# Performance work log

Hardware: AMD Instinct MI355X
Metric: run time of the kernel (lower is better)

The kernel has to match this reference:

```python
import jax, jax.numpy as jnp
import numpy as np

B, S, D, H = 2, 2048, 1024, 16
HD = D // H

def setup_inputs() -> dict:
    key = jax.random.key(0)
    ks = jax.random.split(key, 5)
    sc = 1.0 / np.sqrt(D)
    return {
        "x": jax.random.normal(ks[0], (B, S, D), dtype=jnp.float32),
        "Wq": jax.random.normal(ks[1], (D, D), dtype=jnp.float32) * sc,
        "bq": jnp.zeros((D,), jnp.float32),
        "Wk": jax.random.normal(ks[2], (D, D), dtype=jnp.float32) * sc,
        "bk": jnp.zeros((D,), jnp.float32),
        "Wv": jax.random.normal(ks[3], (D, D), dtype=jnp.float32) * sc,
        "bv": jnp.zeros((D,), jnp.float32),
        "Wo": jax.random.normal(ks[4], (D, D), dtype=jnp.float32) * sc,
        "bo": jnp.zeros((D,), jnp.float32),
    }

def reference(x, Wq, bq, Wk, bk, Wv, bv, Wo, bo):
    b, s, d = x.shape
    def proj(W, bias):
        # [B,S,D] -> [B,H,S,HD]
        return (x @ W + bias).reshape(b, s, H, HD).swapaxes(1, 2)
    q = proj(Wq, bq)
    k = proj(Wk, bk)
    v = proj(Wv, bv)
    # naive full attention, matching the module (materializes [B,H,S,S])
    logits = jnp.einsum("bhqd,bhkd->bhqk", q, k) / jnp.sqrt(jnp.float32(HD))
    attn = jax.nn.softmax(logits, axis=-1)
    vals = jnp.einsum("bhqk,bhkd->bhqd", attn, v)
    vals = vals.swapaxes(1, 2).reshape(b, s, d)
    return vals @ Wo + bo
```

## Files before the change

kernel.cpp:

```cpp
#include <hip/hip_runtime.h>

typedef unsigned short u16;
typedef __bf16 bf16x8 __attribute__((ext_vector_type(8)));
typedef __bf16 bf16x4 __attribute__((ext_vector_type(4)));
typedef float f32x4 __attribute__((ext_vector_type(4)));

#define SC2 0.18033688f

__device__ __forceinline__ u16 f2bf(float f) {
    union { float f; unsigned int i; } v;
    v.f = f;
    unsigned int u = v.i;
    return (u16)((u + 0x7fffu + ((u >> 16) & 1u)) >> 16);
}

__device__ __forceinline__ void dma16(const void* g, void* l) {
    __builtin_amdgcn_global_load_lds(
        (__attribute__((address_space(1))) void*)g,
        (__attribute__((address_space(3))) void*)l, 16, 0, 0);
}


__global__ __launch_bounds__(256) void cvt_w4(
    const float* __restrict__ W0, const float* __restrict__ W1,
    const float* __restrict__ W2, const float* __restrict__ W3,
    u16* __restrict__ out) {
    __shared__ u16 t[32][33];
    int z = blockIdx.z;
    const float* in = (z == 0) ? W0 : (z == 1) ? W1 : (z == 2) ? W2 : W3;
    u16* o = out + (size_t)z * 1048576;
    int bx = blockIdx.x * 32, by = blockIdx.y * 32;
    int tx = threadIdx.x & 31, ty = threadIdx.x >> 5;
#pragma unroll
    for (int i = 0; i < 32; i += 8)
        t[ty + i][tx] = f2bf(in[(size_t)(by + ty + i) * 1024 + bx + tx]);
    __syncthreads();
#pragma unroll
    for (int i = 0; i < 32; i += 8) {
        int n = bx + ty + i, k = by + tx;
        o[(size_t)n * 1024 + (k ^ ((n & 7) << 3))] = t[tx][ty + i];
    }
}

__global__ __launch_bounds__(256) void cvt_x(const float* __restrict__ in,
                                             u16* __restrict__ out) {
    int i = blockIdx.x * 256 + threadIdx.x;
    int s = i >> 8, k = (i & 255) * 4;
    float4 f = reinterpret_cast<const float4*>(in)[i];
    ushort4 h;
    h.x = f2bf(f.x); h.y = f2bf(f.y); h.z = f2bf(f.z); h.w = f2bf(f.w);
    *reinterpret_cast<ushort4*>(&out[(size_t)s * 1024 + (k ^ ((s & 7) << 3))]) = h;
}

__global__ __launch_bounds__(256) void gemm_qkv(
    const u16* __restrict__ xbf, const u16* __restrict__ wt,
    const float* __restrict__ bq, const float* __restrict__ bk,
    const float* __restrict__ bv,
    u16* __restrict__ qkg, u16* __restrict__ vgt) {
    __shared__ __align__(16) u16 As[128 * 64];
    __shared__ __align__(16) u16 Bs[128 * 64];

    int tid = threadIdx.x;
    int m0 = blockIdx.y * 128, n0 = blockIdx.x * 128;
    int wave = tid >> 6, lane = tid & 63;
    int wm = (wave >> 1) * 64, wn = (wave & 1) * 64;
    int l16 = lane & 15, quad = lane >> 4;
    int sl = l16 & 7;

    int seg = n0 >> 10;
    int n0r = n0 & 1023;
    const u16* WT = wt + (size_t)seg * 1048576;
    bool swp = (seg == 2);

    f32x4 acc[4][4];
#pragma unroll
    for (int mi = 0; mi < 4; mi++)
#pragma unroll
        for (int ni = 0; ni < 4; ni++) acc[mi][ni] = (f32x4){0.f, 0.f, 0.f, 0.f};

    int rsub = lane >> 3, c16 = (lane & 7) * 8;
    for (int k0 = 0; k0 < 1024; k0 += 64) {
#pragma unroll
        for (int i = 0; i < 4; i++) {
            int row = wave * 32 + i * 8 + rsub;
            dma16(&xbf[(size_t)(m0 + row) * 1024 + k0 + c16], &As[wave * 2048 + i * 512]);
            dma16(&WT[(size_t)(n0r + row) * 1024 + k0 + c16], &Bs[wave * 2048 + i * 512]);
        }
        __syncthreads();
        const u16* Am = swp ? Bs : As;
        const u16* Bn = swp ? As : Bs;
#pragma unroll
        for (int kk = 0; kk < 64; kk += 32) {
            int co = ((((kk >> 3) + quad) ^ sl) << 3);
            bf16x8 af[4], bf[4];
#pragma unroll
            for (int mi = 0; mi < 4; mi++)
                af[mi] = *reinterpret_cast<const bf16x8*>(
                    &Am[(wm + mi * 16 + l16) * 64 + co]);
#pragma unroll
            for (int ni = 0; ni < 4; ni++)
                bf[ni] = *reinterpret_cast<const bf16x8*>(
                    &Bn[(wn + ni * 16 + l16) * 64 + co]);
#pragma unroll
            for (int mi = 0; mi < 4; mi++)
#pragma unroll
                for (int ni = 0; ni < 4; ni++)
                    acc[mi][ni] = __builtin_amdgcn_mfma_f32_16x16x32_bf16(
                        af[mi], bf[ni], acc[mi][ni], 0, 0, 0);
        }
        __syncthreads();
    }

    if (!swp) {
        float sc = (seg == 0) ? SC2 : 1.0f;
#pragma unroll
        for (int ni = 0; ni < 4; ni++) {
            int n = n0 + wn + ni * 16 + l16;
            float bb = (n < 1024) ? bq[n] : bk[n - 1024];
#pragma unroll
            for (int mi = 0; mi < 4; mi++)
#pragma unroll
                for (int r = 0; r < 4; r++) {
                    int s = m0 + wm + mi * 16 + quad * 4 + r;
                    int key = (seg == 0) ? (s & 7) : ((s >> 2) & 7);
                    int col = n ^ (key << 3);
                    qkg[(size_t)(s >> 11) * 4194304 + (size_t)(s & 2047) * 2048 + col] =
                        f2bf((acc[mi][ni][r] + bb) * sc);
                }
        }
    } else {
#pragma unroll
        for (int mi = 0; mi < 4; mi++)
#pragma unroll
            for (int r = 0; r < 4; r++) {
                int v = n0r + wm + mi * 16 + quad * 4 + r;
                float bb = bv[v];
#pragma unroll
                for (int ni = 0; ni < 4; ni++) {
                    int s = m0 + wn + ni * 16 + l16;
                    int scol = (s & 2047) ^ ((v & 7) << 3);
                    vgt[(size_t)((s >> 11) * 1024 + v) * 2048 + scol] =
                        f2bf(acc[mi][ni][r] + bb);
                }
            }
    }
}

__global__ __launch_bounds__(512) void attention_kern(
    u16* __restrict__ qkg, const u16* __restrict__ vgt) {
    __shared__ __align__(16) u16 KsB[3][64 * 64];
    __shared__ __align__(16) u16 VtB[3][64 * 64];
    __shared__ __align__(16) u16 Ps[128 * 64];

    int tid = threadIdx.x;
    int bid = blockIdx.x;
    int id = (bid & 7) * 64 + (bid >> 3);
    int qt = id & 15, h = (id >> 4) & 15, b = id >> 8;

    int wave = tid >> 6, lane = tid & 63;
    int l16 = lane & 15, quad = lane >> 4;
    int rsub = lane >> 3, c16 = (lane & 7) * 8;
    int sl = l16 & 7;

    u16* qb = qkg + (size_t)b * 4194304 + (size_t)(qt * 128) * 2048 + h * 64;
    const u16* kb = qkg + (size_t)b * 4194304 + 1024 + h * 64;
    const u16* vb = vgt + (size_t)(b * 1024 + h * 64) * 2048;

    bf16x8 qf[2];
    {
        const u16* qr = qb + (size_t)(wave * 16 + l16) * 2048;
        qf[0] = *reinterpret_cast<const bf16x8*>(&qr[(quad ^ sl) << 3]);
        qf[1] = *reinterpret_cast<const bf16x8*>(&qr[((4 + quad) ^ sl) << 3]);
    }

    bf16x8 onef;
#pragma unroll
    for (int i = 0; i < 8; i++) onef[i] = (__bf16)1.0f;

    f32x4 o[4], ls;
#pragma unroll
    for (int ni = 0; ni < 4; ni++) o[ni] = (f32x4){0.f, 0.f, 0.f, 0.f};
    ls = (f32x4){0.f, 0.f, 0.f, 0.f};

    int r8 = wave * 8 + rsub;
    int gk = 4 * (r8 & 15) + (r8 >> 4);

    auto STAGE = [&](int kt, u16* kd, u16* vd) {
        const u16* ktb = kb + (size_t)(kt * 64) * 2048;
        const u16* vtb = vb + kt * 64;
        dma16(&ktb[(size_t)gk * 2048 + c16], kd + wave * 512);
        dma16(&vtb[(size_t)r8 * 2048 + c16], vd + wave * 512);
    };

    u16 *k0 = KsB[0], *k1 = KsB[1], *k2 = KsB[2];
    u16 *v0 = VtB[0], *v1 = VtB[1], *v2 = VtB[2];

    STAGE(0, k0, v0);

    for (int kt = 0; kt < 32; kt++) {
        if (kt < 31) {
            STAGE(kt + 1, k1, v1);
            asm volatile("s_waitcnt vmcnt(2) lgkmcnt(0)\n\ts_barrier" ::: "memory");
        } else {
            asm volatile("s_waitcnt vmcnt(0) lgkmcnt(0)\n\ts_barrier" ::: "memory");
        }

        f32x4 s[4];
#pragma unroll
        for (int ni = 0; ni < 4; ni++) s[ni] = (f32x4){0.f, 0.f, 0.f, 0.f};
#pragma unroll
        for (int kk = 0; kk < 64; kk += 32) {
            int co = ((((kk >> 3) + quad) ^ sl) << 3);
            bf16x8 af = qf[kk >> 5];
#pragma unroll
            for (int ni = 0; ni < 4; ni++) {
                bf16x8 bfr = *reinterpret_cast<const bf16x8*>(
                    &k0[(ni * 16 + l16) * 64 + co]);
                s[ni] = __builtin_amdgcn_mfma_f32_16x16x32_bf16(af, bfr, s[ni], 0, 0, 0);
            }
        }

#pragma unroll
        for (int r = 0; r < 4; r++) {
            f32x4 pf = {__builtin_amdgcn_exp2f(s[0][r]),
                        __builtin_amdgcn_exp2f(s[1][r]),
                        __builtin_amdgcn_exp2f(s[2][r]),
                        __builtin_amdgcn_exp2f(s[3][r])};
            bf16x4 pb = __builtin_convertvector(pf, bf16x4);
            int q = wave * 16 + quad * 4 + r;
            *reinterpret_cast<bf16x4*>(
                &Ps[q * 64 + (((l16 >> 1) ^ (q & 7)) << 3) + (l16 & 1) * 4]) = pb;
        }

#pragma unroll
        for (int kk = 0; kk < 64; kk += 32) {
            int co = ((((kk >> 3) + quad) ^ sl) << 3);
            bf16x8 af = *reinterpret_cast<const bf16x8*>(
                &Ps[(wave * 16 + l16) * 64 + co]);
            ls = __builtin_amdgcn_mfma_f32_16x16x32_bf16(af, onef, ls, 0, 0, 0);
#pragma unroll
            for (int ni = 0; ni < 4; ni++) {
                bf16x8 bfr = *reinterpret_cast<const bf16x8*>(
                    &v0[(ni * 16 + l16) * 64 + co]);
                o[ni] = __builtin_amdgcn_mfma_f32_16x16x32_bf16(af, bfr, o[ni], 0, 0, 0);
            }
        }

        u16* tk = k0; k0 = k1; k1 = k2; k2 = tk;
        u16* tv = v0; v0 = v1; v1 = v2; v2 = tv;
    }

    float inv[4];
#pragma unroll
    for (int r = 0; r < 4; r++) inv[r] = __builtin_amdgcn_rcpf(ls[r]);
#pragma unroll
    for (int ni = 0; ni < 4; ni++)
#pragma unroll
        for (int r = 0; r < 4; r++) {
            int s = qt * 128 + wave * 16 + quad * 4 + r;
            int d = h * 64 + ni * 16 + l16;
            qkg[(size_t)b * 4194304 + (size_t)s * 2048 + (d ^ ((s & 7) << 3))] =
                f2bf(o[ni][r] * inv[r]);
        }
}

__global__ __launch_bounds__(256) void gemm_out(
    const u16* __restrict__ attb, const u16* __restrict__ wot,
    const float* __restrict__ bo, float* __restrict__ out) {
    __shared__ __align__(16) u16 A3[3][128 * 64];
    __shared__ __align__(16) u16 B3[3][64 * 64];

    int tid = threadIdx.x;
    int m0 = blockIdx.y * 128, n0 = blockIdx.x * 64;
    int wave = tid >> 6, lane = tid & 63;
    int wm = (wave >> 1) * 64, wn = (wave & 1) * 32;
    int l16 = lane & 15, quad = lane >> 4;
    int sl = l16 & 7;
    int rsub = lane >> 3, c16 = (lane & 7) * 8;

    f32x4 acc[4][2];
#pragma unroll
    for (int mi = 0; mi < 4; mi++)
#pragma unroll
        for (int ni = 0; ni < 2; ni++) acc[mi][ni] = (f32x4){0.f, 0.f, 0.f, 0.f};

    auto STAGE = [&](int k0, u16* ad, u16* bd) {
#pragma unroll
        for (int i = 0; i < 4; i++) {
            int row = wave * 32 + i * 8 + rsub;
            dma16(&attb[(size_t)(m0 + row) * 2048 + k0 + c16], ad + wave * 2048 + i * 512);
        }
#pragma unroll
        for (int i = 0; i < 2; i++) {
            int row = wave * 16 + i * 8 + rsub;
            dma16(&wot[(size_t)(n0 + row) * 1024 + k0 + c16], bd + wave * 1024 + i * 512);
        }
    };

    u16 *a0 = A3[0], *a1 = A3[1], *a2 = A3[2];
    u16 *b0 = B3[0], *b1 = B3[1], *b2 = B3[2];

    STAGE(0, a0, b0);

    for (int k = 0; k < 16; k++) {
        if (k < 15) {
            STAGE((k + 1) * 64, a1, b1);
            asm volatile("s_waitcnt vmcnt(6) lgkmcnt(0)\n\ts_barrier" ::: "memory");
        } else {
            asm volatile("s_waitcnt vmcnt(0) lgkmcnt(0)\n\ts_barrier" ::: "memory");
        }
#pragma unroll
        for (int kk = 0; kk < 64; kk += 32) {
            int co = ((((kk >> 3) + quad) ^ sl) << 3);
            bf16x8 af[4], bf[2];
#pragma unroll
            for (int mi = 0; mi < 4; mi++)
                af[mi] = *reinterpret_cast<const bf16x8*>(
                    &a0[(wm + mi * 16 + l16) * 64 + co]);
#pragma unroll
            for (int ni = 0; ni < 2; ni++)
                bf[ni] = *reinterpret_cast<const bf16x8*>(
                    &b0[(wn + ni * 16 + l16) * 64 + co]);
#pragma unroll
            for (int mi = 0; mi < 4; mi++)
#pragma unroll
                for (int ni = 0; ni < 2; ni++)
                    acc[mi][ni] = __builtin_amdgcn_mfma_f32_16x16x32_bf16(
                        af[mi], bf[ni], acc[mi][ni], 0, 0, 0);
        }
        u16* t;
        t = a0; a0 = a1; a1 = a2; a2 = t;
        t = b0; b0 = b1; b1 = b2; b2 = t;
    }

#pragma unroll
    for (int ni = 0; ni < 2; ni++) {
        int n = n0 + wn + ni * 16 + l16;
        float bb = bo[n];
#pragma unroll
        for (int mi = 0; mi < 4; mi++)
#pragma unroll
            for (int r = 0; r < 4; r++)
                out[(size_t)(m0 + wm + mi * 16 + quad * 4 + r) * 1024 + n] =
                    acc[mi][ni][r] + bb;
    }
}

extern "C" void kernel_launch(void* const* d_in, const int* in_sizes, int n_in,
                              void* d_out, int out_size, void* d_ws, size_t ws_size,
                              hipStream_t stream) {
    const float* x  = (const float*)d_in[0];
    const float* Wq = (const float*)d_in[1];
    const float* bq = (const float*)d_in[2];
    const float* Wk = (const float*)d_in[3];
    const float* bk = (const float*)d_in[4];
    const float* Wv = (const float*)d_in[5];
    const float* bv = (const float*)d_in[6];
    const float* Wo = (const float*)d_in[7];
    const float* bo = (const float*)d_in[8];

    u16* WT  = (u16*)d_out;
    u16* xbf = (u16*)d_out + 4 * 1048576;
    u16* QKg = (u16*)d_ws;
    u16* Vgt = (u16*)d_ws + 8 * 1048576;

    cvt_w4<<<dim3(32, 32, 4), 256, 0, stream>>>(Wq, Wk, Wv, Wo, WT);
    cvt_x<<<4096, 256, 0, stream>>>(x, xbf);

    gemm_qkv<<<dim3(24, 32), 256, 0, stream>>>(xbf, WT, bq, bk, bv, QKg, Vgt);

    attention_kern<<<dim3(512), 512, 0, stream>>>(QKg, Vgt);

    hipMemcpyAsync(Vgt, WT + 3 * 1048576, (size_t)2 * 1048576,
                   hipMemcpyDeviceToDevice, stream);
    gemm_out<<<dim3(16, 32), 256, 0, stream>>>(QKg, Vgt, bo, (float*)d_out);
}
```

Before: 196.4 us.

## Give each attention wave two 16-row query subtiles to reuse K/V fragments

The attention kernel now launches 256 threads (4 waves) instead of 512, and each wave handles 32 query rows as two 16-row subtiles. The K and V fragments loaded from LDS are reused across both subtiles, which halves LDS reads per MFMA, and each thread issues two DMA loads per stage. The trade-off is more accumulator registers per thread and fewer waves per block to hide latency.

```diff
diff --git a/kernel.cpp b/kernel.cpp
--- a/kernel.cpp
+++ b/kernel.cpp
@@ -146,7 +146,7 @@
     }
 }
 
-__global__ __launch_bounds__(512) void attention_kern(
+__global__ __launch_bounds__(256) void attention_kern(
     u16* __restrict__ qkg, const u16* __restrict__ vgt) {
     __shared__ __align__(16) u16 KsB[3][64 * 64];
     __shared__ __align__(16) u16 VtB[3][64 * 64];
@@ -166,30 +166,36 @@
     const u16* kb = qkg + (size_t)b * 4194304 + 1024 + h * 64;
     const u16* vb = vgt + (size_t)(b * 1024 + h * 64) * 2048;
 
-    bf16x8 qf[2];
-    {
-        const u16* qr = qb + (size_t)(wave * 16 + l16) * 2048;
-        qf[0] = *reinterpret_cast<const bf16x8*>(&qr[(quad ^ sl) << 3]);
-        qf[1] = *reinterpret_cast<const bf16x8*>(&qr[((4 + quad) ^ sl) << 3]);
+    bf16x8 qf[2][2];
+#pragma unroll
+    for (int sub = 0; sub < 2; sub++) {
+        const u16* qr = qb + (size_t)(wave * 32 + sub * 16 + l16) * 2048;
+        qf[sub][0] = *reinterpret_cast<const bf16x8*>(&qr[(quad ^ sl) << 3]);
+        qf[sub][1] = *reinterpret_cast<const bf16x8*>(&qr[((4 + quad) ^ sl) << 3]);
     }
 
     bf16x8 onef;
 #pragma unroll
     for (int i = 0; i < 8; i++) onef[i] = (__bf16)1.0f;
 
-    f32x4 o[4], ls;
-#pragma unroll
-    for (int ni = 0; ni < 4; ni++) o[ni] = (f32x4){0.f, 0.f, 0.f, 0.f};
-    ls = (f32x4){0.f, 0.f, 0.f, 0.f};
-
-    int r8 = wave * 8 + rsub;
-    int gk = 4 * (r8 & 15) + (r8 >> 4);
+    f32x4 o[2][4], ls[2];
+#pragma unroll
+    for (int sub = 0; sub < 2; sub++) {
+        ls[sub] = (f32x4){0.f, 0.f, 0.f, 0.f};
+#pragma unroll
+        for (int ni = 0; ni < 4; ni++) o[sub][ni] = (f32x4){0.f, 0.f, 0.f, 0.f};
+    }
 
     auto STAGE = [&](int kt, u16* kd, u16* vd) {
         const u16* ktb = kb + (size_t)(kt * 64) * 2048;
         const u16* vtb = vb + kt * 64;
-        dma16(&ktb[(size_t)gk * 2048 + c16], kd + wave * 512);
-        dma16(&vtb[(size_t)r8 * 2048 + c16], vd + wave * 512);
+#pragma unroll
+        for (int i = 0; i < 2; i++) {
+            int r8 = (i * 4 + wave) * 8 + rsub;
+            int gk = 4 * (r8 & 15) + (r8 >> 4);
+            dma16(&ktb[(size_t)gk * 2048 + c16], kd + (i * 4 + wave) * 512);
+            dma16(&vtb[(size_t)r8 * 2048 + c16], vd + (i * 4 + wave) * 512);
+        }
     };
 
     u16 *k0 = KsB[0], *k1 = KsB[1], *k2 = KsB[2];
@@ -200,49 +206,64 @@
     for (int kt = 0; kt < 32; kt++) {
         if (kt < 31) {
             STAGE(kt + 1, k1, v1);
-            asm volatile("s_waitcnt vmcnt(2) lgkmcnt(0)\n\ts_barrier" ::: "memory");
+            asm volatile("s_waitcnt vmcnt(4) lgkmcnt(0)\n\ts_barrier" ::: "memory");
         } else {
             asm volatile("s_waitcnt vmcnt(0) lgkmcnt(0)\n\ts_barrier" ::: "memory");
         }
 
-        f32x4 s[4];
-#pragma unroll
-        for (int ni = 0; ni < 4; ni++) s[ni] = (f32x4){0.f, 0.f, 0.f, 0.f};
+        f32x4 s[2][4];
+#pragma unroll
+        for (int sub = 0; sub < 2; sub++)
+#pragma unroll
+            for (int ni = 0; ni < 4; ni++) s[sub][ni] = (f32x4){0.f, 0.f, 0.f, 0.f};
 #pragma unroll
         for (int kk = 0; kk < 64; kk += 32) {
             int co = ((((kk >> 3) + quad) ^ sl) << 3);
-            bf16x8 af = qf[kk >> 5];
-#pragma unroll
-            for (int ni = 0; ni < 4; ni++) {
-                bf16x8 bfr = *reinterpret_cast<const bf16x8*>(
+            bf16x8 kf[4];
+#pragma unroll
+            for (int ni = 0; ni < 4; ni++)
+                kf[ni] = *reinterpret_cast<const bf16x8*>(
                     &k0[(ni * 16 + l16) * 64 + co]);
-                s[ni] = __builtin_amdgcn_mfma_f32_16x16x32_bf16(af, bfr, s[ni], 0, 0, 0);
+#pragma unroll
+            for (int sub = 0; sub < 2; sub++)
+#pragma unroll
+                for (int ni = 0; ni < 4; ni++)
+                    s[sub][ni] = __builtin_amdgcn_mfma_f32_16x16x32_bf16(
+                        qf[sub][kk >> 5], kf[ni], s[sub][ni], 0, 0, 0);
+        }
+
+#pragma unroll
+        for (int sub = 0; sub < 2; sub++)
+#pragma unroll
+            for (int r = 0; r < 4; r++) {
+                f32x4 pf = {__builtin_amdgcn_exp2f(s[sub][0][r]),
+                            __builtin_amdgcn_exp2f(s[sub][1][r]),
+                            __builtin_amdgcn_exp2f(s[sub][2][r]),
+                            __builtin_amdgcn_exp2f(s[sub][3][r])};
+                bf16x4 pb = __builtin_convertvector(pf, bf16x4);
+                int q = wave * 32 + sub * 16 + quad * 4 + r;
+                *reinterpret_cast<bf16x4*>(
+                    &Ps[q * 64 + (((l16 >> 1) ^ (q & 7)) << 3) + (l16 & 1) * 4]) = pb;
             }
-        }
-
-#pragma unroll
-        for (int r = 0; r < 4; r++) {
-            f32x4 pf = {__builtin_amdgcn_exp2f(s[0][r]),
-                        __builtin_amdgcn_exp2f(s[1][r]),
-                        __builtin_amdgcn_exp2f(s[2][r]),
-                        __builtin_amdgcn_exp2f(s[3][r])};
-            bf16x4 pb = __builtin_convertvector(pf, bf16x4);
-            int q = wave * 16 + quad * 4 + r;
-            *reinterpret_cast<bf16x4*>(
-                &Ps[q * 64 + (((l16 >> 1) ^ (q & 7)) << 3) + (l16 & 1) * 4]) = pb;
-        }
 
 #pragma unroll
         for (int kk = 0; kk < 64; kk += 32) {
             int co = ((((kk >> 3) + quad) ^ sl) << 3);
-            bf16x8 af = *reinterpret_cast<const bf16x8*>(
-                &Ps[(wave * 16 + l16) * 64 + co]);
-            ls = __builtin_amdgcn_mfma_f32_16x16x32_bf16(af, onef, ls, 0, 0, 0);
-#pragma unroll
-            for (int ni = 0; ni < 4; ni++) {
-                bf16x8 bfr = *reinterpret_cast<const bf16x8*>(
+            bf16x8 vf[4];
+#pragma unroll
+            for (int ni = 0; ni < 4; ni++)
+                vf[ni] = *reinterpret_cast<const bf16x8*>(
                     &v0[(ni * 16 + l16) * 64 + co]);
-                o[ni] = __builtin_amdgcn_mfma_f32_16x16x32_bf16(af, bfr, o[ni], 0, 0, 0);
+#pragma unroll
+            for (int sub = 0; sub < 2; sub++) {
+                bf16x8 af = *reinterpret_cast<const bf16x8*>(
+                    &Ps[(wave * 32 + sub * 16 + l16) * 64 + co]);
+                ls[sub] = __builtin_amdgcn_mfma_f32_16x16x32_bf16(
+                    af, onef, ls[sub], 0, 0, 0);
+#pragma unroll
+                for (int ni = 0; ni < 4; ni++)
+                    o[sub][ni] = __builtin_amdgcn_mfma_f32_16x16x32_bf16(
+                        af, vf[ni], o[sub][ni], 0, 0, 0);
             }
         }
 
@@ -250,18 +271,21 @@
         u16* tv = v0; v0 = v1; v1 = v2; v2 = tv;
     }
 
-    float inv[4];
-#pragma unroll
-    for (int r = 0; r < 4; r++) inv[r] = __builtin_amdgcn_rcpf(ls[r]);
-#pragma unroll
-    for (int ni = 0; ni < 4; ni++)
-#pragma unroll
-        for (int r = 0; r < 4; r++) {
-            int s = qt * 128 + wave * 16 + quad * 4 + r;
-            int d = h * 64 + ni * 16 + l16;
-            qkg[(size_t)b * 4194304 + (size_t)s * 2048 + (d ^ ((s & 7) << 3))] =
-                f2bf(o[ni][r] * inv[r]);
-        }
+#pragma unroll
+    for (int sub = 0; sub < 2; sub++) {
+        float inv[4];
+#pragma unroll
+        for (int r = 0; r < 4; r++) inv[r] = __builtin_amdgcn_rcpf(ls[sub][r]);
+#pragma unroll
+        for (int ni = 0; ni < 4; ni++)
+#pragma unroll
+            for (int r = 0; r < 4; r++) {
+                int s = qt * 128 + wave * 32 + sub * 16 + quad * 4 + r;
+                int d = h * 64 + ni * 16 + l16;
+                qkg[(size_t)b * 4194304 + (size_t)s * 2048 + (d ^ ((s & 7) << 3))] =
+                    f2bf(o[sub][ni][r] * inv[r]);
+            }
+    }
 }
 
 __global__ __launch_bounds__(256) void gemm_out(
@@ -369,7 +393,7 @@
 
     gemm_qkv<<<dim3(24, 32), 256, 0, stream>>>(xbf, WT, bq, bk, bv, QKg, Vgt);
 
-    attention_kern<<<dim3(512), 512, 0, stream>>>(QKg, Vgt);
+    attention_kern<<<dim3(512), 256, 0, stream>>>(QKg, Vgt);
 
     hipMemcpyAsync(Vgt, WT + 3 * 1048576, (size_t)2 * 1048576,
                    hipMemcpyDeviceToDevice, stream);
```

Measured after the change: 203.6 us. +3.7%, slower.
